# Performance work log

Hardware: AMD Instinct MI355X
Metric: run time of the kernel (lower is better)

The kernel has to match this reference:

```python
import jax, jax.numpy as jnp
import numpy as np

B, J, C = 8, 2048, 256
K = 32
H = 8
D = 32  # out_dim per head


def setup_inputs() -> dict:
    key = jax.random.key(0)
    k0, k1, k2, k3, k4, k5 = jax.random.split(key, 6)
    x = jax.random.normal(k0, (B, J, C), dtype=jnp.float32)
    nbr_idx = jax.random.randint(k1, (B, J, K), 0, J)
    s_in = 1.0 / np.sqrt(C)
    s_hd = 1.0 / np.sqrt(H * D)
    Wq = jax.random.uniform(k2, (C, H * D), dtype=jnp.float32, minval=-s_in, maxval=s_in)
    Wk = jax.random.uniform(k3, (C, H * D), dtype=jnp.float32, minval=-s_in, maxval=s_in)
    Wv = jax.random.uniform(k4, (C, H * D), dtype=jnp.float32, minval=-s_in, maxval=s_in)
    Wp = jax.random.uniform(k5, (H * D, D), dtype=jnp.float32, minval=-s_hd, maxval=s_hd)
    return {"x": x, "nbr_idx": nbr_idx, "Wq": Wq, "Wk": Wk, "Wv": Wv, "Wp": Wp}


def reference(x, nbr_idx, Wq, Wk, Wv, Wp):
    b, j, c = x.shape
    q = (x @ Wq).reshape(b, j, H, D)  # [B,J,H,D]
    k = (x @ Wk).reshape(b, j, H, D)
    v = (x @ Wv).reshape(b, j, H, D)
    bidx = jnp.arange(b)[:, None, None]  # [B,1,1]
    k_nbr = k[bidx, nbr_idx]  # [B,J,K,H,D]
    v_nbr = v[bidx, nbr_idx]  # [B,J,K,H,D]
    attn = jnp.einsum("bjhd,bjkhd->bjkh", q, k_nbr) / np.sqrt(D)
    attn = jax.nn.leaky_relu(attn, negative_slope=0.2)
    attn = jax.nn.softmax(attn, axis=2)  # softmax over K neighbors
    out = jnp.einsum("bjkh,bjkhd->bjhd", attn, v_nbr).reshape(b, j, H * D)
    return out @ Wp  # [B,J,D]
```

## Files before the change

### kernel.cpp

```cpp
#include <hip/hip_runtime.h>
#include <hip/hip_bf16.h>


typedef short bf16x8 __attribute__((ext_vector_type(8)));
typedef float f32x4  __attribute__((ext_vector_type(4)));
typedef float f32x2  __attribute__((ext_vector_type(2)));
typedef _Float16 h16x2 __attribute__((ext_vector_type(2)));

__device__ __forceinline__ float bf2f(unsigned short u) {
    union { unsigned int i; float f; } c; c.i = ((unsigned int)u) << 16; return c.f;
}
__device__ __forceinline__ unsigned short f2bf(float f) {
    union { float f; unsigned int i; } c; c.f = f;
    unsigned int r = c.i + 0x7FFFu + ((c.i >> 16) & 1u);
    return (unsigned short)(r >> 16);
}
__device__ __forceinline__ unsigned short f2h(float f) {
    union { _Float16 h; unsigned short u; } c; c.h = (_Float16)f;
    return c.u;
}
__device__ __forceinline__ f32x2 upk(unsigned int u) {
    union { unsigned int i; float f; } lo, hi;
    lo.i = u << 16;
    hi.i = u & 0xffff0000u;
    return (f32x2){lo.f, hi.f};
}

#if defined(__has_builtin)
#if __has_builtin(__builtin_amdgcn_fdot2)
#define HAVE_FDOT2 1
#endif
#endif
__device__ __forceinline__ float dot2acc(unsigned int a, unsigned int b, float acc) {
#ifdef HAVE_FDOT2
    union { unsigned int u; h16x2 v; } ca, cb;
    ca.u = a; cb.u = b;
    return __builtin_amdgcn_fdot2(ca.v, cb.v, acc, false);
#else
    union { unsigned int u; _Float16 h[2]; } ca, cb;
    ca.u = a; cb.u = b;
    return acc + (float)ca.h[0] * (float)cb.h[0] + (float)ca.h[1] * (float)cb.h[1];
#endif
}

__device__ __forceinline__ void gld_lds16(void* lds, const void* g) {
    __builtin_amdgcn_global_load_lds(
        (const __attribute__((address_space(1))) unsigned int*)g,
        (__attribute__((address_space(3))) unsigned int*)lds,
        16, 0, 0);
}

__global__ __launch_bounds__(256) void prep(
    const float* __restrict__ x,
    const float* __restrict__ Wq, const float* __restrict__ Wk,
    const float* __restrict__ Wv, const float* __restrict__ Wp,
    unsigned short* __restrict__ xb, unsigned short* __restrict__ Wt)
{
    const int blk = blockIdx.x, tid = threadIdx.x;
    if (blk < 4096) {
        int t = blk * 256 + tid;
        float4 f = ((const float4*)x)[t];
        ushort4 u;
        u.x = f2bf(f.x); u.y = f2bf(f.y); u.z = f2bf(f.z); u.w = f2bf(f.w);
        ((ushort4*)xb)[t] = u;
        return;
    }
    int wi = blk - 4096;
    int w = wi >> 8, n = wi & 255, t = tid;
    if (w == 0) {
        Wt[(size_t)n * 256 + t] = f2bf(Wq[(size_t)t * 256 + n]);
    } else if (w == 1) {
        Wt[(size_t)(256 + n) * 256 + t] = f2bf(Wk[(size_t)t * 256 + n]);
    } else {
        int h = n >> 5, c = n & 31;
        float acc = 0.f;
#pragma unroll
        for (int d = 0; d < 32; d++)
            acc += Wv[(size_t)t * 256 + h * 32 + d] * Wp[(size_t)(h * 32 + d) * 32 + c];
        Wt[(size_t)(512 + n) * 256 + t] = f2bf(acc);
    }
}

__global__ __launch_bounds__(256) void qkv_mfma(
    const unsigned short* __restrict__ xb,
    const unsigned short* __restrict__ Wt,
    unsigned short* __restrict__ Q, unsigned short* __restrict__ Kp,
    unsigned short* __restrict__ VP)
{
    __shared__ unsigned short Als[128][64];
    __shared__ unsigned short Bls[128][64];

    const unsigned short* Wb = Wt + (size_t)blockIdx.z * 65536;
    unsigned short* Y = (blockIdx.z == 0) ? Q : (blockIdx.z == 1) ? Kp : VP;
    const bool as_f16 = (blockIdx.z != 2);

    const int row0 = blockIdx.x * 128;
    const int col0 = blockIdx.y * 128;
    const int tid  = threadIdx.x;
    const int w    = tid >> 6, l = tid & 63;
    const int wm   = (w >> 1) * 64, wn = (w & 1) * 64;
    const int lm   = l & 15, quad = l >> 4;

    f32x4 acc[4][4];
#pragma unroll
    for (int i = 0; i < 4; i++)
#pragma unroll
        for (int j = 0; j < 4; j++) acc[i][j] = (f32x4){0.f, 0.f, 0.f, 0.f};

    const char* Ab = (const char*)(xb + (size_t)row0 * 256);
    const char* Bb = (const char*)(Wb + (size_t)col0 * 256);

    for (int k0 = 0; k0 < 256; k0 += 64) {
#pragma unroll
        for (int i = 0; i < 4; i++) {
            int s = i * 256 + tid;
            int r = s >> 3, c = s & 7;
            size_t go = (size_t)r * 512 + (size_t)k0 * 2 + c * 16;
            gld_lds16((char*)Als + s * 16, Ab + go);
            gld_lds16((char*)Bls + s * 16, Bb + go);
        }
        __syncthreads();

#pragma unroll
        for (int kk = 0; kk < 64; kk += 32) {
            bf16x8 a[4], b[4];
#pragma unroll
            for (int tm = 0; tm < 4; tm++)
                a[tm] = *(const bf16x8*)&Als[wm + tm * 16 + lm][kk + quad * 8];
#pragma unroll
            for (int tn = 0; tn < 4; tn++)
                b[tn] = *(const bf16x8*)&Bls[wn + tn * 16 + lm][kk + quad * 8];
#pragma unroll
            for (int tm = 0; tm < 4; tm++)
#pragma unroll
                for (int tn = 0; tn < 4; tn++)
                    acc[tm][tn] = __builtin_amdgcn_mfma_f32_16x16x32_bf16(
                        a[tm], b[tn], acc[tm][tn], 0, 0, 0);
        }
        __syncthreads();
    }

#pragma unroll
    for (int tm = 0; tm < 4; tm++) {
        int rbase = row0 + wm + tm * 16 + quad * 4;
#pragma unroll
        for (int tn = 0; tn < 4; tn++) {
            int col = col0 + wn + tn * 16 + lm;
            if (as_f16) {
#pragma unroll
                for (int r = 0; r < 4; r++)
                    Y[(size_t)(rbase + r) * 256 + col] = f2h(acc[tm][tn][r]);
            } else {
#pragma unroll
                for (int r = 0; r < 4; r++)
                    Y[(size_t)(rbase + r) * 256 + col] = f2bf(acc[tm][tn][r]);
            }
        }
    }
}

__global__ __launch_bounds__(256) void attn_all(
    const unsigned short* __restrict__ qb,
    const unsigned short* __restrict__ kb,
    const unsigned short* __restrict__ vp,
    const int*            __restrict__ nbr,
    float*                __restrict__ out)
{
    __shared__ float sc[8 * 33];
    __shared__ float pw[8 * 33];
    __shared__ float redB[8 * 264];
    __shared__ float red2[256];

    const int b   = blockIdx.x & 7;
    const int j   = blockIdx.x >> 3;
    const int bj  = (b << 11) + j;
    const int tid = threadIdx.x;

    const int w    = tid >> 6;
    const int l    = tid & 63;
    const int lh   = l & 31;
    const int half = l >> 5;
    const int hA   = lh >> 2;
    const int g    = 2 * w + half;
    const size_t bbase = (size_t)b << 19;
    const int* nrow = nbr + (size_t)bj * 32;

    uint4 qu = *(const uint4*)(qb + (size_t)bj * 256 + lh * 8);

    int koA[4], koB[4];
#pragma unroll
    for (int p = 0; p < 4; p++) koA[p] = nrow[w * 8 + 2 * p + half] << 8;
#pragma unroll
    for (int p = 0; p < 4; p++) koB[p] = nrow[p * 8 + g] << 8;

    uint4 ku[4], vu[4];
#pragma unroll
    for (int p = 0; p < 4; p++)
        ku[p] = *(const uint4*)(kb + bbase + koA[p] + lh * 8);
#pragma unroll
    for (int p = 0; p < 4; p++)
        vu[p] = *(const uint4*)(vp + bbase + koB[p] + lh * 8);

#pragma unroll
    for (int p = 0; p < 4; p++) {
        const int kkA = w * 8 + 2 * p + half;
        float acc = 0.f;
        acc = dot2acc(ku[p].x, qu.x, acc);
        acc = dot2acc(ku[p].y, qu.y, acc);
        acc = dot2acc(ku[p].z, qu.z, acc);
        acc = dot2acc(ku[p].w, qu.w, acc);
        acc += __shfl_xor(acc, 1);
        acc += __shfl_xor(acc, 2);
        if ((l & 3) == 0) {
            float s = acc * 0.17677669529663687f;
            s = (s > 0.f) ? s : 0.2f * s;
            sc[hA * 33 + kkA] = s;
        }
    }
    __syncthreads();

    {
        const int h2  = 2 * w + half;
        const int kk2 = lh;
        float s = sc[h2 * 33 + kk2];
        float mx = s;
#pragma unroll
        for (int m = 16; m >= 1; m >>= 1) mx = fmaxf(mx, __shfl_xor(mx, m));
        float e = __expf(s - mx);
        float sum = e;
#pragma unroll
        for (int m = 16; m >= 1; m >>= 1) sum += __shfl_xor(sum, m);
        pw[h2 * 33 + kk2] = e / sum;
    }
    __syncthreads();

    {
        f32x2 a0 = (f32x2){0.f,0.f}, a1 = a0, a2v = a0, a3 = a0;
#pragma unroll
        for (int p = 0; p < 4; p++) {
            const int kkB = p * 8 + g;
            const float wgt = pw[hA * 33 + kkB];
            const f32x2 w2 = (f32x2){wgt, wgt};
            a0  += upk(vu[p].x) * w2;
            a1  += upk(vu[p].y) * w2;
            a2v += upk(vu[p].z) * w2;
            a3  += upk(vu[p].w) * w2;
        }
        float* rb = &redB[g * 264 + lh * 8];
        *(float4*)(rb)     = make_float4(a0.x, a0.y, a1.x, a1.y);
        *(float4*)(rb + 4) = make_float4(a2v.x, a2v.y, a3.x, a3.y);
    }
    __syncthreads();

    {
        float s = 0.f;
#pragma unroll
        for (int gg = 0; gg < 8; gg++) s += redB[gg * 264 + tid];
        red2[tid] = s;
    }
    __syncthreads();

    if (tid < 32) {
        float o = 0.f;
#pragma unroll
        for (int h = 0; h < 8; h++) o += red2[h * 32 + tid];
        out[(size_t)bj * 32 + tid] = o;
    }
}

__global__ __launch_bounds__(256) void fused_all(
    const float* __restrict__ X, const int* __restrict__ nbr,
    const float* __restrict__ Wq, const float* __restrict__ Wk,
    const float* __restrict__ Wv, const float* __restrict__ Wp,
    float* __restrict__ out)
{
    __shared__ float xr[256], qrow[256], xn[256];
    __shared__ float vn[32][256];
    __shared__ int   nb[32];
    __shared__ float sc[32][8], pwv[32][8];
    __shared__ float sp[256], hd[256];
    __shared__ float red[8][32];

    const int bj = blockIdx.x, b = bj >> 11, tid = threadIdx.x;

    xr[tid] = X[(size_t)bj * 256 + tid];
    if (tid < 32) nb[tid] = nbr[(size_t)bj * 32 + tid];
    __syncthreads();

    {
        float acc = 0.f;
#pragma unroll 8
        for (int c = 0; c < 256; c++) acc += xr[c] * Wq[(size_t)c * 256 + tid];
        qrow[tid] = acc;
    }
    __syncthreads();

    for (int i = 0; i < 32; i++) {
        size_t r = (size_t)(b * 2048 + nb[i]);
        xn[tid] = X[r * 256 + tid];
        __syncthreads();
        float ka = 0.f, va = 0.f;
#pragma unroll 8
        for (int c = 0; c < 256; c++) {
            float xc = xn[c];
            ka += xc * Wk[(size_t)c * 256 + tid];
            va += xc * Wv[(size_t)c * 256 + tid];
        }
        vn[i][tid] = va;
        sp[tid] = qrow[tid] * ka;
        __syncthreads();
        if (tid < 8) {
            float s = 0.f;
#pragma unroll
            for (int d = 0; d < 32; d++) s += sp[tid * 32 + d];
            s *= 0.17677669529663687f;
            s = (s > 0.f) ? s : 0.2f * s;
            sc[i][tid] = s;
        }
        __syncthreads();
    }

    {
        const int h = tid & 7, kk = tid >> 3;
        float mx = -1e30f;
#pragma unroll
        for (int i = 0; i < 32; i++) mx = fmaxf(mx, sc[i][h]);
        float ssum = 0.f;
#pragma unroll
        for (int i = 0; i < 32; i++) ssum += __expf(sc[i][h] - mx);
        pwv[kk][h] = __expf(sc[kk][h] - mx) / ssum;
    }
    __syncthreads();

    {
        const int h2 = tid >> 5;
        float acc = 0.f;
#pragma unroll 8
        for (int i = 0; i < 32; i++) acc += pwv[i][h2] * vn[i][tid];
        hd[tid] = acc;
    }
    __syncthreads();

    {
        const int c = tid & 31, ch = tid >> 5;
        float p = 0.f;
#pragma unroll
        for (int i = 0; i < 32; i++) { int r = ch * 32 + i; p += hd[r] * Wp[r * 32 + c]; }
        red[ch][c] = p;
    }
    __syncthreads();

    if (tid < 32) {
        float o = 0.f;
#pragma unroll
        for (int i = 0; i < 8; i++) o += red[i][tid];
        out[(size_t)bj * 32 + tid] = o;
    }
}

extern "C" void kernel_launch(void* const* d_in, const int* in_sizes, int n_in,
                              void* d_out, int out_size, void* d_ws, size_t ws_size,
                              hipStream_t stream) {
    const float* x   = (const float*)d_in[0];
    const int*   nbr = (const int*)d_in[1];
    const float* Wq  = (const float*)d_in[2];
    const float* Wk  = (const float*)d_in[3];
    const float* Wv  = (const float*)d_in[4];
    const float* Wp  = (const float*)d_in[5];
    float*       out = (float*)d_out;

    const size_t ME   = (size_t)16384 * 256;
    const size_t need = (4 * ME + 3 * 65536) * sizeof(unsigned short);

    if (ws_size >= need) {
        unsigned short* q  = (unsigned short*)d_ws;
        unsigned short* k  = q + ME;
        unsigned short* vp = k + ME;
        unsigned short* xb = vp + ME;
        unsigned short* Wt = xb + ME;

        prep<<<4096 + 768, 256, 0, stream>>>(x, Wq, Wk, Wv, Wp, xb, Wt);
        qkv_mfma<<<dim3(128, 2, 3), 256, 0, stream>>>(xb, Wt, q, k, vp);
        attn_all<<<16384, 256, 0, stream>>>(q, k, vp, nbr, out);
    } else {
        fused_all<<<16384, 256, 0, stream>>>(x, nbr, Wq, Wk, Wv, Wp, out);
    }
}
```

Measured before the change: 123.0 us.

## Process one query row per wavefront with register-only softmax and shuffle reduction

The attention kernel now assigns one (batch, row) to each 64-lane wavefront instead of one row per 256-thread block. Each half-wave covers 16 of the 32 neighbors. Scores, softmax and the weighted V sum stay in registers, and the cross-lane reductions use shuffles, so the shared-memory staging and the four block-wide barriers are gone. Each lane now holds 16 K and 16 V vectors, which raises register pressure and may lower occupancy.

```diff
diff --git a/kernel.cpp b/kernel.cpp
--- a/kernel.cpp
+++ b/kernel.cpp
@@ -159,112 +159,92 @@
     }
 }
 
-__global__ __launch_bounds__(256) void attn_all(
+__global__ __launch_bounds__(256) void attn_wave(
     const unsigned short* __restrict__ qb,
     const unsigned short* __restrict__ kb,
     const unsigned short* __restrict__ vp,
     const int*            __restrict__ nbr,
     float*                __restrict__ out)
 {
-    __shared__ float sc[8 * 33];
-    __shared__ float pw[8 * 33];
-    __shared__ float redB[8 * 264];
-    __shared__ float red2[256];
-
-    const int b   = blockIdx.x & 7;
-    const int j   = blockIdx.x >> 3;
-    const int bj  = (b << 11) + j;
-    const int tid = threadIdx.x;
-
+    const int beta = blockIdx.x;
+    const int b    = beta & 7;
+    const int jt   = beta >> 3;
+    const int tid  = threadIdx.x;
     const int w    = tid >> 6;
     const int l    = tid & 63;
     const int lh   = l & 31;
-    const int half = l >> 5;
-    const int hA   = lh >> 2;
-    const int g    = 2 * w + half;
+    const int h5   = l >> 5;
+    const int bj   = (b << 11) + jt * 4 + w;
     const size_t bbase = (size_t)b << 19;
     const int* nrow = nbr + (size_t)bj * 32;
 
+    int ko = nrow[lh] << 8;
+    int koff[16];
+#pragma unroll
+    for (int r = 0; r < 16; r++) koff[r] = __shfl(ko, 2 * r + h5);
+
     uint4 qu = *(const uint4*)(qb + (size_t)bj * 256 + lh * 8);
 
-    int koA[4], koB[4];
-#pragma unroll
-    for (int p = 0; p < 4; p++) koA[p] = nrow[w * 8 + 2 * p + half] << 8;
-#pragma unroll
-    for (int p = 0; p < 4; p++) koB[p] = nrow[p * 8 + g] << 8;
-
-    uint4 ku[4], vu[4];
-#pragma unroll
-    for (int p = 0; p < 4; p++)
-        ku[p] = *(const uint4*)(kb + bbase + koA[p] + lh * 8);
-#pragma unroll
-    for (int p = 0; p < 4; p++)
-        vu[p] = *(const uint4*)(vp + bbase + koB[p] + lh * 8);
-
-#pragma unroll
-    for (int p = 0; p < 4; p++) {
-        const int kkA = w * 8 + 2 * p + half;
-        float acc = 0.f;
-        acc = dot2acc(ku[p].x, qu.x, acc);
-        acc = dot2acc(ku[p].y, qu.y, acc);
-        acc = dot2acc(ku[p].z, qu.z, acc);
-        acc = dot2acc(ku[p].w, qu.w, acc);
-        acc += __shfl_xor(acc, 1);
-        acc += __shfl_xor(acc, 2);
-        if ((l & 3) == 0) {
-            float s = acc * 0.17677669529663687f;
-            s = (s > 0.f) ? s : 0.2f * s;
-            sc[hA * 33 + kkA] = s;
-        }
-    }
-    __syncthreads();
-
-    {
-        const int h2  = 2 * w + half;
-        const int kk2 = lh;
-        float s = sc[h2 * 33 + kk2];
-        float mx = s;
-#pragma unroll
-        for (int m = 16; m >= 1; m >>= 1) mx = fmaxf(mx, __shfl_xor(mx, m));
-        float e = __expf(s - mx);
-        float sum = e;
-#pragma unroll
-        for (int m = 16; m >= 1; m >>= 1) sum += __shfl_xor(sum, m);
-        pw[h2 * 33 + kk2] = e / sum;
-    }
-    __syncthreads();
-
-    {
-        f32x2 a0 = (f32x2){0.f,0.f}, a1 = a0, a2v = a0, a3 = a0;
-#pragma unroll
-        for (int p = 0; p < 4; p++) {
-            const int kkB = p * 8 + g;
-            const float wgt = pw[hA * 33 + kkB];
-            const f32x2 w2 = (f32x2){wgt, wgt};
-            a0  += upk(vu[p].x) * w2;
-            a1  += upk(vu[p].y) * w2;
-            a2v += upk(vu[p].z) * w2;
-            a3  += upk(vu[p].w) * w2;
-        }
-        float* rb = &redB[g * 264 + lh * 8];
-        *(float4*)(rb)     = make_float4(a0.x, a0.y, a1.x, a1.y);
-        *(float4*)(rb + 4) = make_float4(a2v.x, a2v.y, a3.x, a3.y);
-    }
-    __syncthreads();
-
-    {
-        float s = 0.f;
-#pragma unroll
-        for (int gg = 0; gg < 8; gg++) s += redB[gg * 264 + tid];
-        red2[tid] = s;
-    }
-    __syncthreads();
-
-    if (tid < 32) {
-        float o = 0.f;
-#pragma unroll
-        for (int h = 0; h < 8; h++) o += red2[h * 32 + tid];
-        out[(size_t)bj * 32 + tid] = o;
+    uint4 kr[16];
+#pragma unroll
+    for (int r = 0; r < 16; r++)
+        kr[r] = *(const uint4*)(kb + bbase + koff[r] + lh * 8);
+
+    float s[16];
+#pragma unroll
+    for (int r = 0; r < 16; r++) {
+        float a = 0.f;
+        a = dot2acc(kr[r].x, qu.x, a);
+        a = dot2acc(kr[r].y, qu.y, a);
+        a = dot2acc(kr[r].z, qu.z, a);
+        a = dot2acc(kr[r].w, qu.w, a);
+        a += __shfl_xor(a, 1);
+        a += __shfl_xor(a, 2);
+        a *= 0.17677669529663687f;
+        s[r] = (a > 0.f) ? a : 0.2f * a;
+    }
+
+    uint4 vr[16];
+#pragma unroll
+    for (int r = 0; r < 16; r++)
+        vr[r] = *(const uint4*)(vp + bbase + koff[r] + lh * 8);
+
+    float m = s[0];
+#pragma unroll
+    for (int r = 1; r < 16; r++) m = fmaxf(m, s[r]);
+    m = fmaxf(m, __shfl_xor(m, 32));
+    float sum = 0.f;
+#pragma unroll
+    for (int r = 0; r < 16; r++) { s[r] = __expf(s[r] - m); sum += s[r]; }
+    sum += __shfl_xor(sum, 32);
+    const float inv = 1.0f / sum;
+#pragma unroll
+    for (int r = 0; r < 16; r++) s[r] *= inv;
+
+    f32x2 a0 = (f32x2){0.f, 0.f}, a1 = a0, a2 = a0, a3 = a0;
+#pragma unroll
+    for (int r = 0; r < 16; r++) {
+        const f32x2 w2 = (f32x2){s[r], s[r]};
+        a0 += upk(vr[r].x) * w2;
+        a1 += upk(vr[r].y) * w2;
+        a2 += upk(vr[r].z) * w2;
+        a3 += upk(vr[r].w) * w2;
+    }
+
+    float o[8] = {a0.x, a0.y, a1.x, a1.y, a2.x, a2.y, a3.x, a3.y};
+#pragma unroll
+    for (int i = 0; i < 8; i++) o[i] += __shfl_xor(o[i], 32);
+#pragma unroll
+    for (int i = 0; i < 8; i++) o[i] += __shfl_xor(o[i], 4);
+#pragma unroll
+    for (int i = 0; i < 8; i++) o[i] += __shfl_xor(o[i], 8);
+#pragma unroll
+    for (int i = 0; i < 8; i++) o[i] += __shfl_xor(o[i], 16);
+
+    if (l < 4) {
+        float* op = out + (size_t)bj * 32 + l * 8;
+        *(float4*)(op)     = make_float4(o[0], o[1], o[2], o[3]);
+        *(float4*)(op + 4) = make_float4(o[4], o[5], o[6], o[7]);
     }
 }
 
@@ -381,7 +361,7 @@
 
         prep<<<4096 + 768, 256, 0, stream>>>(x, Wq, Wk, Wv, Wp, xb, Wt);
         qkv_mfma<<<dim3(128, 2, 3), 256, 0, stream>>>(xb, Wt, q, k, vp);
-        attn_all<<<16384, 256, 0, stream>>>(q, k, vp, nbr, out);
+        attn_wave<<<4096, 256, 0, stream>>>(q, k, vp, nbr, out);
     } else {
         fused_all<<<16384, 256, 0, stream>>>(x, nbr, Wq, Wk, Wv, Wp, out);
     }
```

New measurement: 119.3 us. -3.0%, faster.
